# Kernel tuning notes

Measured on AMD Instinct MI355X. Metric: run time of the kernel, lower is better.

## Reference

```python
import jax, jax.numpy as jnp
import numpy as np

T, D_IN, D_OUT, R, S = 8192, 4096, 4096, 16, 16  # tokens, in, out, lora rank, n_stacks
GATE_THRESHOLD = 0.12


def setup_inputs() -> dict:
    key = jax.random.key(0)
    ks = jax.random.split(key, 6)
    x = jax.random.normal(ks[0], (T, D_IN), jnp.float32)
    W = jax.random.normal(ks[1], (D_OUT, D_IN), jnp.float32) * 0.02  # frozen linear weight
    b = jax.random.normal(ks[2], (D_OUT,), jnp.float32) * 0.02       # frozen linear bias
    A = jax.random.normal(ks[3], (S, R, D_IN), jnp.float32) * 0.02   # per-stack lora_A
    B = jax.random.normal(ks[4], (S, D_OUT, R), jnp.float32) * 0.02  # per-stack lora_B
    domain_weights = jax.random.uniform(ks[5], (S,), jnp.float32)    # sigmoid-router weights per domain
    stack_domain = jnp.arange(S, dtype=jnp.int32)                    # stack -> domain index (count=1 each)
    return {"x": x, "W": W, "b": b, "A": A, "B": B,
            "domain_weights": domain_weights, "stack_domain": stack_domain}


def reference(x, W, b, A, B, domain_weights, stack_domain):
    # base frozen linear: out = x @ W^T + b
    base = x @ W.T + b  # [T, D_OUT]
    # threshold-gated per-stack weights: w if w > GATE_THRESHOLD else 0
    g = jnp.where(domain_weights > GATE_THRESHOLD, domain_weights, 0.0)[stack_domain]  # [S]
    # grouped LoRA: stack(x) = (x @ A_s^T) @ B_s^T, combined with gate weights
    h = jnp.einsum('td,srd->str', x, A)          # [S, T, R]
    lora = jnp.einsum('s,str,sor->to', g, h, B)  # [T, D_OUT]
    # original wraps stack contributions in torch.no_grad()
    return base + jax.lax.stop_gradient(lora)
```

## Files before the change

### kernel.cpp

```cpp
#include <hip/hip_runtime.h>
#include <hip/hip_bf16.h>

typedef __bf16 bf16;
typedef __attribute__((ext_vector_type(8))) __bf16 bf16x8;
typedef __attribute__((ext_vector_type(4))) float f32x4;

#define T_TOK 8192
#define DIN   4096
#define DOUT  4096
#define RNK   16
#define NS    16
#define KLORA (NS * RNK)
#define GATE  0.12f

typedef __attribute__((address_space(1))) const void gconst_t;
typedef __attribute__((address_space(3))) void lds_t;

__device__ __forceinline__ void gload_lds16(const void* g, void* l) {
  __builtin_amdgcn_global_load_lds((gconst_t*)g, (lds_t*)l, 16, 0, 0);
}

#define BAR() do { asm volatile("" ::: "memory"); \
                   __builtin_amdgcn_s_barrier();  \
                   asm volatile("" ::: "memory"); } while (0)
#define VMW(n) asm volatile("s_waitcnt vmcnt(" #n ")" ::: "memory")
#define LGKM(n) do { asm volatile("s_waitcnt lgkmcnt(" #n ")" ::: "memory"); \
                     __builtin_amdgcn_sched_barrier(0); } while (0)
#define SB0 __builtin_amdgcn_sched_barrier(0)

__global__ __launch_bounds__(256)
void prep_all_kernel(const float* __restrict__ x, bf16* __restrict__ xb,
                     const float* __restrict__ B, const float* __restrict__ dw,
                     const int* __restrict__ sd, bf16* __restrict__ bg,
                     const float* __restrict__ A, bf16* __restrict__ at) {
  __shared__ float tl[32][33];
  const int bid = blockIdx.x;
  if (bid < 16384) {
    const long i = ((long)bid * 256 + threadIdx.x) * 8;
    const float4 v0 = *(const float4*)(x + i);
    const float4 v1 = *(const float4*)(x + i + 4);
    bf16x8 o;
    o[0] = (bf16)v0.x; o[1] = (bf16)v0.y; o[2] = (bf16)v0.z; o[3] = (bf16)v0.w;
    o[4] = (bf16)v1.x; o[5] = (bf16)v1.y; o[6] = (bf16)v1.z; o[7] = (bf16)v1.w;
    *(bf16x8*)(xb + i) = o;
  } else if (bid < 16384 + 4096) {
    const int t = (bid - 16384) * 256 + threadIdx.x;
    const int o = t >> 8, k = t & 255, s = k >> 4, r = k & 15;
    const float w = dw[sd[s]];
    const float g = (w > GATE) ? w : 0.f;
    bg[t] = (bf16)(g * B[((size_t)s * DOUT + o) * RNK + r]);
  } else {
    const int tb = bid - 16384 - 4096;
    const int d0 = (tb & 127) * 32, k0 = (tb >> 7) * 32;
    const int tx = threadIdx.x & 31, ty = threadIdx.x >> 5;
#pragma unroll
    for (int i = 0; i < 32; i += 8)
      tl[ty + i][tx] = A[(size_t)(k0 + ty + i) * DIN + d0 + tx];
    __syncthreads();
#pragma unroll
    for (int i = 0; i < 32; i += 8)
      at[(size_t)(d0 + ty + i) * KLORA + k0 + tx] = (bf16)tl[tx][ty + i];
  }
}

__global__ __launch_bounds__(256)
void gemm_bt(const bf16* __restrict__ Am, const bf16* __restrict__ Bm,
             const float* __restrict__ extra, bf16* __restrict__ outB,
             int M, int N, int K) {
  constexpr int BM = 128, BN = 128, BK = 32;
  __shared__ __align__(16) bf16 At[BM * BK];
  __shared__ __align__(16) bf16 Bt[BN * BK];

  const int tid  = threadIdx.x;
  const int wave = tid >> 6, lane = tid & 63;

  const int nwg = gridDim.x, bid = blockIdx.x;
  const int qq  = nwg >> 3;
  const int sw  = (bid & 7) * qq + (bid >> 3);
  const int ntN = N / BN;
  const long row0 = (long)(sw / ntN) * BM;
  const long col0 = (long)(sw % ntN) * BN;

  f32x4 acc[4][4] = {};
  const int kSteps = K / BK;

  auto stage = [&](int ks) {
    const long k0 = (long)ks * BK;
#pragma unroll
    for (int r = 0; r < 2; ++r) {
      const int off = tid * 16 + r * 4096;
      const int row = off >> 6;
      const int el  = (off & 63) >> 1;
      char* ldsA = (char*)At + (wave << 10) + (r << 12);
      char* ldsB = (char*)Bt + (wave << 10) + (r << 12);
      gload_lds16(Am + (row0 + row) * K + k0 + el, ldsA);
      gload_lds16(Bm + (col0 + row) * K + k0 + el, ldsB);
    }
  };

  stage(0);
  for (int ks = 0; ks < kSteps; ++ks) {
    __syncthreads();
    bf16x8 afr[4], bfr[4];
    const int koff = (lane >> 4) << 3;
    const int rsel = lane & 15;
    const int wr = wave >> 1, wc = wave & 1;
#pragma unroll
    for (int m = 0; m < 4; ++m)
      afr[m] = *(const bf16x8*)&At[((wr << 6) + (m << 4) + rsel) * BK + koff];
#pragma unroll
    for (int n = 0; n < 4; ++n)
      bfr[n] = *(const bf16x8*)&Bt[((wc << 6) + (n << 4) + rsel) * BK + koff];
    __syncthreads();
    if (ks + 1 < kSteps) stage(ks + 1);
#pragma unroll
    for (int m = 0; m < 4; ++m)
#pragma unroll
      for (int n = 0; n < 4; ++n)
        acc[m][n] = __builtin_amdgcn_mfma_f32_16x16x32_bf16(afr[m], bfr[n],
                                                            acc[m][n], 0, 0, 0);
  }

  const int wr = wave >> 1, wc = wave & 1;
#pragma unroll
  for (int m = 0; m < 4; ++m)
#pragma unroll
    for (int n = 0; n < 4; ++n)
#pragma unroll
      for (int j = 0; j < 4; ++j) {
        const long row = row0 + wr * 64 + m * 16 + ((lane >> 4) << 2) + j;
        const long col = col0 + wc * 64 + n * 16 + (lane & 15);
        outB[row * N + col] = (bf16)(acc[m][n][j] + extra[row * N + col]);
      }
}

__global__ __launch_bounds__(512, 2)
void gemm256(const bf16* __restrict__ Am, const bf16* __restrict__ Bm,
             const float* __restrict__ bias, float* __restrict__ out,
             int M, int N, int K) {
  extern __shared__ char smem[];
  const int tid  = threadIdx.x;
  const int wave = tid >> 6, lane = tid & 63;
  const int wr = wave >> 2, wc = wave & 3;
  const int rsel = lane & 15, klane = lane >> 4;

  const int nwg = gridDim.x, bid = blockIdx.x;
  const int sw  = (bid & 7) * (nwg >> 3) + (bid >> 3);
  const int ntN = N >> 8;
  const long row0 = (long)(sw / ntN) << 8;
  const long col0 = (long)(sw % ntN) << 8;

  long srcA[2], srcB[2];
  int  ldsd[2];
  {
    const int rlo = lane >> 2;
    const int kbe = (((lane & 3) * 16) ^ (((lane >> 5) & 1) << 5)) >> 1;
#pragma unroll
    for (int r = 0; r < 2; ++r) {
      const int row = wave * 32 + r * 16 + rlo;
      srcA[r] = (row0 + row) * (long)K + kbe;
      srcB[r] = (col0 + row) * (long)K + kbe;
      ldsd[r] = (wave * 2 + r) << 10;
    }
  }

  const int nT = K >> 6;

  auto stage_half = [&](int H) {
    if (H >= 4 * nT) return;
    const int  slot = H & 7;
    const long kofs = (long)(H >> 2) * 64 + (long)((H >> 1) & 1) * 32;
    if (H & 1) {
#pragma unroll
      for (int r = 0; r < 2; ++r)
        gload_lds16(Bm + srcB[r] + kofs, smem + (slot << 14) + ldsd[r]);
    } else {
#pragma unroll
      for (int r = 0; r < 2; ++r)
        gload_lds16(Am + srcA[r] + kofs, smem + (slot << 14) + ldsd[r]);
    }
  };

  const int laneoff = rsel * 64 + ((klane * 16) ^ ((rsel & 8) << 2));

  f32x4 acc[8][4] = {};
  bf16x8 afr0[4], afr1[4], bfr0[4], bfr1[4];

#define RDA(slot, mh, mi, dst) \
  (dst)[(mi)] = *(const bf16x8*)(smem + ((slot) << 14) + \
                 (((wr << 7) + (mh) * 64 + (mi) * 16) << 6) + laneoff)
#define RDB(slot, n, dst) \
  (dst)[(n)] = *(const bf16x8*)(smem + ((slot) << 14) + \
                (((wc << 6) + (n) * 16) << 6) + laneoff)
#define MB(mh, mi, A_, B_) do { \
  acc[(mh)*4+(mi)][0] = __builtin_amdgcn_mfma_f32_16x16x32_bf16((A_)[(mi)], (B_)[0], acc[(mh)*4+(mi)][0], 0, 0, 0); \
  acc[(mh)*4+(mi)][1] = __builtin_amdgcn_mfma_f32_16x16x32_bf16((A_)[(mi)], (B_)[1], acc[(mh)*4+(mi)][1], 0, 0, 0); \
  acc[(mh)*4+(mi)][2] = __builtin_amdgcn_mfma_f32_16x16x32_bf16((A_)[(mi)], (B_)[2], acc[(mh)*4+(mi)][2], 0, 0, 0); \
  acc[(mh)*4+(mi)][3] = __builtin_amdgcn_mfma_f32_16x16x32_bf16((A_)[(mi)], (B_)[3], acc[(mh)*4+(mi)][3], 0, 0, 0); \
} while (0)

  stage_half(0); stage_half(1); stage_half(2); stage_half(3); stage_half(4);
  VMW(6);
  BAR();
  RDB(1, 0, bfr0); RDB(1, 1, bfr0); RDB(1, 2, bfr0); RDB(1, 3, bfr0);
  RDA(0, 0, 0, afr0); RDA(0, 0, 1, afr0); RDA(0, 0, 2, afr0); RDA(0, 0, 3, afr0);

  for (int t = 0; t < nT; ++t) {
    const int b  = (t & 1) << 2;
    const int b2 = b ^ 4;
    const bool last = (t == nT - 1);
    BAR();
    stage_half(4 * t + 5);
    LGKM(0);
    __builtin_amdgcn_s_setprio(1);
    MB(0, 0, afr0, bfr0); SB0; RDA(b | 0, 1, 0, afr1); SB0;
    MB(0, 1, afr0, bfr0); SB0; RDA(b | 0, 1, 1, afr1); SB0;
    MB(0, 2, afr0, bfr0); SB0; RDA(b | 0, 1, 2, afr1); SB0;
    MB(0, 3, afr0, bfr0); SB0; RDA(b | 0, 1, 3, afr1);
    __builtin_amdgcn_s_setprio(0);
    if (last) { VMW(0); } else { VMW(4); }
    BAR();
    stage_half(4 * t + 6);
    LGKM(0);
    __builtin_amdgcn_s_setprio(1);
    MB(1, 0, afr1, bfr0); SB0; RDB(b | 3, 0, bfr1); RDB(b | 3, 1, bfr1); SB0;
    MB(1, 1, afr1, bfr0); SB0; RDB(b | 3, 2, bfr1); RDB(b | 3, 3, bfr1); SB0;
    MB(1, 2, afr1, bfr0); SB0; RDA(b | 2, 0, 0, afr0); RDA(b | 2, 0, 1, afr0); SB0;
    MB(1, 3, afr1, bfr0); SB0; RDA(b | 2, 0, 2, afr0); RDA(b | 2, 0, 3, afr0);
    __builtin_amdgcn_s_setprio(0);
    BAR();
    stage_half(4 * t + 7);
    LGKM(0);
    __builtin_amdgcn_s_setprio(1);
    MB(0, 0, afr0, bfr1); SB0; RDA(b | 2, 1, 0, afr1); SB0;
    MB(0, 1, afr0, bfr1); SB0; RDA(b | 2, 1, 1, afr1); SB0;
    MB(0, 2, afr0, bfr1); SB0; RDA(b | 2, 1, 2, afr1); SB0;
    MB(0, 3, afr0, bfr1); SB0; RDA(b | 2, 1, 3, afr1);
    __builtin_amdgcn_s_setprio(0);
    VMW(4);
    BAR();
    stage_half(4 * t + 8);
    LGKM(0);
    __builtin_amdgcn_s_setprio(1);
    if (!last) {
      MB(1, 0, afr1, bfr1); SB0; RDB(b2 | 1, 0, bfr0); RDB(b2 | 1, 1, bfr0); SB0;
      MB(1, 1, afr1, bfr1); SB0; RDB(b2 | 1, 2, bfr0); RDB(b2 | 1, 3, bfr0); SB0;
      MB(1, 2, afr1, bfr1); SB0; RDA(b2 | 0, 0, 0, afr0); RDA(b2 | 0, 0, 1, afr0); SB0;
      MB(1, 3, afr1, bfr1); SB0; RDA(b2 | 0, 0, 2, afr0); RDA(b2 | 0, 0, 3, afr0);
    } else {
      MB(1, 0, afr1, bfr1); MB(1, 1, afr1, bfr1);
      MB(1, 2, afr1, bfr1); MB(1, 3, afr1, bfr1);
    }
    __builtin_amdgcn_s_setprio(0);
  }

#undef RDA
#undef RDB
#undef MB

#pragma unroll
  for (int m = 0; m < 8; ++m)
#pragma unroll
    for (int n = 0; n < 4; ++n)
#pragma unroll
      for (int j = 0; j < 4; ++j) {
        const long row = row0 + wr * 128 + m * 16 + klane * 4 + j;
        const long col = col0 + wc * 64 + n * 16 + rsel;
        out[row * N + col] = acc[m][n][j] + bias[col];
      }
}


extern "C" void kernel_launch(void* const* d_in, const int* in_sizes, int n_in,
                              void* d_out, int out_size, void* d_ws, size_t ws_size,
                              hipStream_t stream) {
  (void)in_sizes; (void)n_in; (void)out_size; (void)ws_size;
  const float* x  = (const float*)d_in[0];
  const float* W  = (const float*)d_in[1];
  const float* b  = (const float*)d_in[2];
  const float* A  = (const float*)d_in[3];
  const float* B  = (const float*)d_in[4];
  const float* dw = (const float*)d_in[5];
  const int*   sd = (const int*)d_in[6];
  float* out = (float*)d_out;

  char* ws = (char*)d_ws;
  bf16* xb    = (bf16*)(ws);
  bf16* weff  = (bf16*)(ws + ((size_t)64 << 20));
  bf16* bg    = (bf16*)(ws + ((size_t)96 << 20));
  bf16* acatT = (bf16*)(ws + ((size_t)98 << 20));

  prep_all_kernel<<<16384 + 4096 + 1024, 256, 0, stream>>>(
      x, xb, B, dw, sd, bg, A, acatT);

  gemm_bt<<<(DOUT / 128) * (DIN / 128), 256, 0, stream>>>(
      bg, acatT, W, weff, DOUT, DIN, KLORA);

  static_assert((T_TOK % 256) == 0 && (DOUT % 256) == 0 && (DIN % 64) == 0, "");
  hipFuncSetAttribute(reinterpret_cast<const void*>(gemm256),
                      hipFuncAttributeMaxDynamicSharedMemorySize, 131072);
  gemm256<<<(T_TOK / 256) * (DOUT / 256), 512, 131072, stream>>>(
      xb, weff, b, out, T_TOK, DOUT, DIN);
}
```

Baseline: 324.5 us.

## Switch main GEMM from 16x16x32 to 32x32x16 bf16 MFMA tiles

Replaces the 16x16x32 MFMA instruction tiling of the 256x256 GEMM with 32x32x16 MFMAs. The LDS swizzle, fragment reads and epilogue indexing are changed to match the 32-row fragment layout. Larger MFMA tiles need fewer LDS fragment reads per FLOP and fewer instructions, which should ease LDS bandwidth and issue pressure. The new swizzle could cause bank conflicts or produce wrong results if it does not match the staging layout.

```diff
diff --git a/kernel.cpp b/kernel.cpp
--- a/kernel.cpp
+++ b/kernel.cpp
@@ -4,6 +4,7 @@
 typedef __bf16 bf16;
 typedef __attribute__((ext_vector_type(8))) __bf16 bf16x8;
 typedef __attribute__((ext_vector_type(4))) float f32x4;
+typedef __attribute__((ext_vector_type(16))) float f32x16;
 
 #define T_TOK 8192
 #define DIN   4096
@@ -142,7 +143,7 @@
   const int tid  = threadIdx.x;
   const int wave = tid >> 6, lane = tid & 63;
   const int wr = wave >> 2, wc = wave & 3;
-  const int rsel = lane & 15, klane = lane >> 4;
+  const int lane31 = lane & 31, kh = lane >> 5;
 
   const int nwg = gridDim.x, bid = blockIdx.x;
   const int sw  = (bid & 7) * (nwg >> 3) + (bid >> 3);
@@ -152,16 +153,13 @@
 
   long srcA[2], srcB[2];
   int  ldsd[2];
-  {
-    const int rlo = lane >> 2;
-    const int kbe = (((lane & 3) * 16) ^ (((lane >> 5) & 1) << 5)) >> 1;
-#pragma unroll
-    for (int r = 0; r < 2; ++r) {
-      const int row = wave * 32 + r * 16 + rlo;
-      srcA[r] = (row0 + row) * (long)K + kbe;
-      srcB[r] = (col0 + row) * (long)K + kbe;
-      ldsd[r] = (wave * 2 + r) << 10;
-    }
+#pragma unroll
+  for (int r = 0; r < 2; ++r) {
+    const int row = wave * 32 + r * 16 + (lane >> 2);
+    const int kbe = ((((lane & 3) * 16) ^ ((lane & 32) >> 1) ^ (r << 5)) >> 1);
+    srcA[r] = (row0 + row) * (long)K + kbe;
+    srcB[r] = (col0 + row) * (long)K + kbe;
+    ldsd[r] = (wave * 2 + r) << 10;
   }
 
   const int nT = K >> 6;
@@ -181,29 +179,31 @@
     }
   };
 
-  const int laneoff = rsel * 64 + ((klane * 16) ^ ((rsel & 8) << 2));
-
-  f32x4 acc[8][4] = {};
-  bf16x8 afr0[4], afr1[4], bfr0[4], bfr1[4];
-
-#define RDA(slot, mh, mi, dst) \
-  (dst)[(mi)] = *(const bf16x8*)(smem + ((slot) << 14) + \
-                 (((wr << 7) + (mh) * 64 + (mi) * 16) << 6) + laneoff)
-#define RDB(slot, n, dst) \
-  (dst)[(n)] = *(const bf16x8*)(smem + ((slot) << 14) + \
-                (((wc << 6) + (n) * 16) << 6) + laneoff)
-#define MB(mh, mi, A_, B_) do { \
-  acc[(mh)*4+(mi)][0] = __builtin_amdgcn_mfma_f32_16x16x32_bf16((A_)[(mi)], (B_)[0], acc[(mh)*4+(mi)][0], 0, 0, 0); \
-  acc[(mh)*4+(mi)][1] = __builtin_amdgcn_mfma_f32_16x16x32_bf16((A_)[(mi)], (B_)[1], acc[(mh)*4+(mi)][1], 0, 0, 0); \
-  acc[(mh)*4+(mi)][2] = __builtin_amdgcn_mfma_f32_16x16x32_bf16((A_)[(mi)], (B_)[2], acc[(mh)*4+(mi)][2], 0, 0, 0); \
-  acc[(mh)*4+(mi)][3] = __builtin_amdgcn_mfma_f32_16x16x32_bf16((A_)[(mi)], (B_)[3], acc[(mh)*4+(mi)][3], 0, 0, 0); \
-} while (0)
+  const int swz = (lane & 24) << 1;
+  int lo32[2];
+  lo32[0] = lane31 * 64 + (((0 * 2 + kh) * 16) ^ swz);
+  lo32[1] = lane31 * 64 + (((1 * 2 + kh) * 16) ^ swz);
+
+  f32x16 acc32[4][2] = {};
+  bf16x8 afr0[2][2], afr1[2][2], bfr0[2][2], bfr1[2][2];
+
+#define RDA32(slot, mh, mi, kst, dst) \
+  (dst)[(mi)][(kst)] = *(const bf16x8*)(smem + ((slot) << 14) + \
+      (((wr << 7) + (mh) * 64 + (mi) * 32) << 6) + lo32[(kst)])
+#define RDB32(slot, n, kst, dst) \
+  (dst)[(n)][(kst)] = *(const bf16x8*)(smem + ((slot) << 14) + \
+      (((wc << 6) + (n) * 32) << 6) + lo32[(kst)])
+#define MB32(mh, mi, n, kst, A_, B_) \
+  acc32[(mh) * 2 + (mi)][(n)] = __builtin_amdgcn_mfma_f32_32x32x16_bf16( \
+      (A_)[(mi)][(kst)], (B_)[(n)][(kst)], acc32[(mh) * 2 + (mi)][(n)], 0, 0, 0)
 
   stage_half(0); stage_half(1); stage_half(2); stage_half(3); stage_half(4);
   VMW(6);
   BAR();
-  RDB(1, 0, bfr0); RDB(1, 1, bfr0); RDB(1, 2, bfr0); RDB(1, 3, bfr0);
-  RDA(0, 0, 0, afr0); RDA(0, 0, 1, afr0); RDA(0, 0, 2, afr0); RDA(0, 0, 3, afr0);
+  RDB32(1, 0, 0, bfr0); RDB32(1, 0, 1, bfr0);
+  RDB32(1, 1, 0, bfr0); RDB32(1, 1, 1, bfr0);
+  RDA32(0, 0, 0, 0, afr0); RDA32(0, 0, 0, 1, afr0);
+  RDA32(0, 0, 1, 0, afr0); RDA32(0, 0, 1, 1, afr0);
 
   for (int t = 0; t < nT; ++t) {
     const int b  = (t & 1) << 2;
@@ -213,29 +213,29 @@
     stage_half(4 * t + 5);
     LGKM(0);
     __builtin_amdgcn_s_setprio(1);
-    MB(0, 0, afr0, bfr0); SB0; RDA(b | 0, 1, 0, afr1); SB0;
-    MB(0, 1, afr0, bfr0); SB0; RDA(b | 0, 1, 1, afr1); SB0;
-    MB(0, 2, afr0, bfr0); SB0; RDA(b | 0, 1, 2, afr1); SB0;
-    MB(0, 3, afr0, bfr0); SB0; RDA(b | 0, 1, 3, afr1);
+    MB32(0, 0, 0, 0, afr0, bfr0); MB32(0, 0, 1, 0, afr0, bfr0); SB0; RDA32(b | 0, 1, 0, 0, afr1); SB0;
+    MB32(0, 1, 0, 0, afr0, bfr0); MB32(0, 1, 1, 0, afr0, bfr0); SB0; RDA32(b | 0, 1, 1, 0, afr1); SB0;
+    MB32(0, 0, 0, 1, afr0, bfr0); MB32(0, 0, 1, 1, afr0, bfr0); SB0; RDA32(b | 0, 1, 0, 1, afr1); SB0;
+    MB32(0, 1, 0, 1, afr0, bfr0); MB32(0, 1, 1, 1, afr0, bfr0); SB0; RDA32(b | 0, 1, 1, 1, afr1);
     __builtin_amdgcn_s_setprio(0);
     if (last) { VMW(0); } else { VMW(4); }
     BAR();
     stage_half(4 * t + 6);
     LGKM(0);
     __builtin_amdgcn_s_setprio(1);
-    MB(1, 0, afr1, bfr0); SB0; RDB(b | 3, 0, bfr1); RDB(b | 3, 1, bfr1); SB0;
-    MB(1, 1, afr1, bfr0); SB0; RDB(b | 3, 2, bfr1); RDB(b | 3, 3, bfr1); SB0;
-    MB(1, 2, afr1, bfr0); SB0; RDA(b | 2, 0, 0, afr0); RDA(b | 2, 0, 1, afr0); SB0;
-    MB(1, 3, afr1, bfr0); SB0; RDA(b | 2, 0, 2, afr0); RDA(b | 2, 0, 3, afr0);
+    MB32(1, 0, 0, 0, afr1, bfr0); MB32(1, 0, 1, 0, afr1, bfr0); SB0; RDB32(b | 3, 0, 0, bfr1); RDB32(b | 3, 0, 1, bfr1); SB0;
+    MB32(1, 1, 0, 0, afr1, bfr0); MB32(1, 1, 1, 0, afr1, bfr0); SB0; RDB32(b | 3, 1, 0, bfr1); RDB32(b | 3, 1, 1, bfr1); SB0;
+    MB32(1, 0, 0, 1, afr1, bfr0); MB32(1, 0, 1, 1, afr1, bfr0); SB0; RDA32(b | 2, 0, 0, 0, afr0); RDA32(b | 2, 0, 0, 1, afr0); SB0;
+    MB32(1, 1, 0, 1, afr1, bfr0); MB32(1, 1, 1, 1, afr1, bfr0); SB0; RDA32(b | 2, 0, 1, 0, afr0); RDA32(b | 2, 0, 1, 1, afr0);
     __builtin_amdgcn_s_setprio(0);
     BAR();
     stage_half(4 * t + 7);
     LGKM(0);
     __builtin_amdgcn_s_setprio(1);
-    MB(0, 0, afr0, bfr1); SB0; RDA(b | 2, 1, 0, afr1); SB0;
-    MB(0, 1, afr0, bfr1); SB0; RDA(b | 2, 1, 1, afr1); SB0;
-    MB(0, 2, afr0, bfr1); SB0; RDA(b | 2, 1, 2, afr1); SB0;
-    MB(0, 3, afr0, bfr1); SB0; RDA(b | 2, 1, 3, afr1);
+    MB32(0, 0, 0, 0, afr0, bfr1); MB32(0, 0, 1, 0, afr0, bfr1); SB0; RDA32(b | 2, 1, 0, 0, afr1); SB0;
+    MB32(0, 1, 0, 0, afr0, bfr1); MB32(0, 1, 1, 0, afr0, bfr1); SB0; RDA32(b | 2, 1, 1, 0, afr1); SB0;
+    MB32(0, 0, 0, 1, afr0, bfr1); MB32(0, 0, 1, 1, afr0, bfr1); SB0; RDA32(b | 2, 1, 0, 1, afr1); SB0;
+    MB32(0, 1, 0, 1, afr0, bfr1); MB32(0, 1, 1, 1, afr0, bfr1); SB0; RDA32(b | 2, 1, 1, 1, afr1);
     __builtin_amdgcn_s_setprio(0);
     VMW(4);
     BAR();
@@ -243,30 +243,32 @@
     LGKM(0);
     __builtin_amdgcn_s_setprio(1);
     if (!last) {
-      MB(1, 0, afr1, bfr1); SB0; RDB(b2 | 1, 0, bfr0); RDB(b2 | 1, 1, bfr0); SB0;
-      MB(1, 1, afr1, bfr1); SB0; RDB(b2 | 1, 2, bfr0); RDB(b2 | 1, 3, bfr0); SB0;
-      MB(1, 2, afr1, bfr1); SB0; RDA(b2 | 0, 0, 0, afr0); RDA(b2 | 0, 0, 1, afr0); SB0;
-      MB(1, 3, afr1, bfr1); SB0; RDA(b2 | 0, 0, 2, afr0); RDA(b2 | 0, 0, 3, afr0);
+      MB32(1, 0, 0, 0, afr1, bfr1); MB32(1, 0, 1, 0, afr1, bfr1); SB0; RDB32(b2 | 1, 0, 0, bfr0); RDB32(b2 | 1, 0, 1, bfr0); SB0;
+      MB32(1, 1, 0, 0, afr1, bfr1); MB32(1, 1, 1, 0, afr1, bfr1); SB0; RDB32(b2 | 1, 1, 0, bfr0); RDB32(b2 | 1, 1, 1, bfr0); SB0;
+      MB32(1, 0, 0, 1, afr1, bfr1); MB32(1, 0, 1, 1, afr1, bfr1); SB0; RDA32(b2 | 0, 0, 0, 0, afr0); RDA32(b2 | 0, 0, 0, 1, afr0); SB0;
+      MB32(1, 1, 0, 1, afr1, bfr1); MB32(1, 1, 1, 1, afr1, bfr1); SB0; RDA32(b2 | 0, 0, 1, 0, afr0); RDA32(b2 | 0, 0, 1, 1, afr0);
     } else {
-      MB(1, 0, afr1, bfr1); MB(1, 1, afr1, bfr1);
-      MB(1, 2, afr1, bfr1); MB(1, 3, afr1, bfr1);
+      MB32(1, 0, 0, 0, afr1, bfr1); MB32(1, 0, 1, 0, afr1, bfr1);
+      MB32(1, 1, 0, 0, afr1, bfr1); MB32(1, 1, 1, 0, afr1, bfr1);
+      MB32(1, 0, 0, 1, afr1, bfr1); MB32(1, 0, 1, 1, afr1, bfr1);
+      MB32(1, 1, 0, 1, afr1, bfr1); MB32(1, 1, 1, 1, afr1, bfr1);
     }
     __builtin_amdgcn_s_setprio(0);
   }
 
-#undef RDA
-#undef RDB
-#undef MB
-
-#pragma unroll
-  for (int m = 0; m < 8; ++m)
-#pragma unroll
-    for (int n = 0; n < 4; ++n)
-#pragma unroll
-      for (int j = 0; j < 4; ++j) {
-        const long row = row0 + wr * 128 + m * 16 + klane * 4 + j;
-        const long col = col0 + wc * 64 + n * 16 + rsel;
-        out[row * N + col] = acc[m][n][j] + bias[col];
+#undef RDA32
+#undef RDB32
+#undef MB32
+
+#pragma unroll
+  for (int mi4 = 0; mi4 < 4; ++mi4)
+#pragma unroll
+    for (int n = 0; n < 2; ++n)
+#pragma unroll
+      for (int reg = 0; reg < 16; ++reg) {
+        const long row = row0 + wr * 128 + mi4 * 32 + (reg & 3) + ((reg >> 2) << 3) + (kh << 2);
+        const long col = col0 + wc * 64 + n * 32 + lane31;
+        out[row * N + col] = acc32[mi4][n][reg] + bias[col];
       }
 }
 
```

Result: no change. 325.6 us (+0.3%).

## Shrink main GEMM tile to 256x128 with triple-buffered K=32 pipeline

Applied to the files above, without the earlier changes.

The main bf16 GEMM moves from a 256x256 output tile with 8 LDS half-slots and a hand-interleaved four-phase schedule to a 256x128 tile. It now uses a 3-stage ring of K=32 slices in 72KB of LDS and a simpler two-phase loop per slice. The smaller LDS and register footprint is meant to raise occupancy (launch bounds 4) and double the number of workgroups. The cost is lower arithmetic intensity per tile, more global traffic for the A operand, more barriers per unit of K, and loss of the finely interleaved MFMA/ds_read scheduling.

```diff
diff --git a/kernel.cpp b/kernel.cpp
--- a/kernel.cpp
+++ b/kernel.cpp
@@ -134,7 +134,7 @@
       }
 }
 
-__global__ __launch_bounds__(512, 2)
+__global__ __launch_bounds__(512, 4)
 void gemm256(const bf16* __restrict__ Am, const bf16* __restrict__ Bm,
              const float* __restrict__ bias, float* __restrict__ out,
              int M, int N, int K) {
@@ -146,112 +146,78 @@
 
   const int nwg = gridDim.x, bid = blockIdx.x;
   const int sw  = (bid & 7) * (nwg >> 3) + (bid >> 3);
-  const int ntN = N >> 8;
+  const int ntN = N >> 7;
   const long row0 = (long)(sw / ntN) << 8;
-  const long col0 = (long)(sw % ntN) << 8;
-
-  long srcA[2], srcB[2];
-  int  ldsd[2];
-  {
-    const int rlo = lane >> 2;
-    const int kbe = (((lane & 3) * 16) ^ (((lane >> 5) & 1) << 5)) >> 1;
-#pragma unroll
-    for (int r = 0; r < 2; ++r) {
-      const int row = wave * 32 + r * 16 + rlo;
-      srcA[r] = (row0 + row) * (long)K + kbe;
-      srcB[r] = (col0 + row) * (long)K + kbe;
-      ldsd[r] = (wave * 2 + r) << 10;
-    }
-  }
-
-  const int nT = K >> 6;
-
-  auto stage_half = [&](int H) {
-    if (H >= 4 * nT) return;
-    const int  slot = H & 7;
-    const long kofs = (long)(H >> 2) * 64 + (long)((H >> 1) & 1) * 32;
-    if (H & 1) {
-#pragma unroll
-      for (int r = 0; r < 2; ++r)
-        gload_lds16(Bm + srcB[r] + kofs, smem + (slot << 14) + ldsd[r]);
-    } else {
-#pragma unroll
-      for (int r = 0; r < 2; ++r)
-        gload_lds16(Am + srcA[r] + kofs, smem + (slot << 14) + ldsd[r]);
-    }
+  const long col0 = (long)(sw % ntN) << 7;
+
+  long srcA[2];
+  int  ldsdA[2];
+#pragma unroll
+  for (int r = 0; r < 2; ++r) {
+    const int row = wave * 32 + r * 16 + (lane >> 2);
+    const int kbe = ((((lane & 3) * 16) ^ (lane & 32)) >> 1);
+    srcA[r] = (row0 + row) * (long)K + kbe;
+    ldsdA[r] = (wave * 2 + r) << 10;
+  }
+  const int rowB = tid >> 2;
+  const int kbeB = ((((lane & 3) * 16) ^ (lane & 32)) >> 1);
+  const long srcB = (col0 + rowB) * (long)K + kbeB;
+  const int  ldsdB = wave << 10;
+
+  const int nS = K >> 5;
+
+  auto stageA = [&](int p, int s2) {
+#pragma unroll
+    for (int r = 0; r < 2; ++r)
+      gload_lds16(Am + srcA[r] + (long)s2 * 32, smem + p * 24576 + ldsdA[r]);
   };
+  auto stageB = [&](int p, int s2) {
+    gload_lds16(Bm + srcB + (long)s2 * 32, smem + p * 24576 + 16384 + ldsdB);
+  };
 
   const int laneoff = rsel * 64 + ((klane * 16) ^ ((rsel & 8) << 2));
 
-  f32x4 acc[8][4] = {};
-  bf16x8 afr0[4], afr1[4], bfr0[4], bfr1[4];
-
-#define RDA(slot, mh, mi, dst) \
-  (dst)[(mi)] = *(const bf16x8*)(smem + ((slot) << 14) + \
-                 (((wr << 7) + (mh) * 64 + (mi) * 16) << 6) + laneoff)
-#define RDB(slot, n, dst) \
-  (dst)[(n)] = *(const bf16x8*)(smem + ((slot) << 14) + \
-                (((wc << 6) + (n) * 16) << 6) + laneoff)
-#define MB(mh, mi, A_, B_) do { \
-  acc[(mh)*4+(mi)][0] = __builtin_amdgcn_mfma_f32_16x16x32_bf16((A_)[(mi)], (B_)[0], acc[(mh)*4+(mi)][0], 0, 0, 0); \
-  acc[(mh)*4+(mi)][1] = __builtin_amdgcn_mfma_f32_16x16x32_bf16((A_)[(mi)], (B_)[1], acc[(mh)*4+(mi)][1], 0, 0, 0); \
-  acc[(mh)*4+(mi)][2] = __builtin_amdgcn_mfma_f32_16x16x32_bf16((A_)[(mi)], (B_)[2], acc[(mh)*4+(mi)][2], 0, 0, 0); \
-  acc[(mh)*4+(mi)][3] = __builtin_amdgcn_mfma_f32_16x16x32_bf16((A_)[(mi)], (B_)[3], acc[(mh)*4+(mi)][3], 0, 0, 0); \
-} while (0)
-
-  stage_half(0); stage_half(1); stage_half(2); stage_half(3); stage_half(4);
-  VMW(6);
+  f32x4 acc[8][2] = {};
+  bf16x8 afr[4], bfr[2];
+
+#define RDA(p, mi, j) \
+  afr[(j)] = *(const bf16x8*)(smem + (p) * 24576 + \
+      (((wr << 7) + (mi) * 16) << 6) + laneoff)
+#define RDB(p, n) \
+  bfr[(n)] = *(const bf16x8*)(smem + (p) * 24576 + 16384 + \
+      (((wc << 5) + (n) * 16) << 6) + laneoff)
+#define MB(mi, j, n) \
+  acc[(mi)][(n)] = __builtin_amdgcn_mfma_f32_16x16x32_bf16( \
+      afr[(j)], bfr[(n)], acc[(mi)][(n)], 0, 0, 0)
+
+  stageB(0, 0); stageA(0, 0);
+  stageB(1, 1); stageA(1, 1);
+  VMW(3);
   BAR();
-  RDB(1, 0, bfr0); RDB(1, 1, bfr0); RDB(1, 2, bfr0); RDB(1, 3, bfr0);
-  RDA(0, 0, 0, afr0); RDA(0, 0, 1, afr0); RDA(0, 0, 2, afr0); RDA(0, 0, 3, afr0);
-
-  for (int t = 0; t < nT; ++t) {
-    const int b  = (t & 1) << 2;
-    const int b2 = b ^ 4;
-    const bool last = (t == nT - 1);
+
+  int p = 0, pst = 2;
+  for (int s = 0; s < nS; ++s) {
+    const bool more = (s + 2 < nS);
+    RDB(p, 0); RDB(p, 1);
+    RDA(p, 0, 0); RDA(p, 1, 1); RDA(p, 2, 2); RDA(p, 3, 3);
+    if (more) stageB(pst, s + 2);
     BAR();
-    stage_half(4 * t + 5);
     LGKM(0);
     __builtin_amdgcn_s_setprio(1);
-    MB(0, 0, afr0, bfr0); SB0; RDA(b | 0, 1, 0, afr1); SB0;
-    MB(0, 1, afr0, bfr0); SB0; RDA(b | 0, 1, 1, afr1); SB0;
-    MB(0, 2, afr0, bfr0); SB0; RDA(b | 0, 1, 2, afr1); SB0;
-    MB(0, 3, afr0, bfr0); SB0; RDA(b | 0, 1, 3, afr1);
+    MB(0, 0, 0); MB(0, 0, 1); MB(1, 1, 0); MB(1, 1, 1);
+    MB(2, 2, 0); MB(2, 2, 1); MB(3, 3, 0); MB(3, 3, 1);
     __builtin_amdgcn_s_setprio(0);
-    if (last) { VMW(0); } else { VMW(4); }
+    RDA(p, 4, 0); RDA(p, 5, 1); RDA(p, 6, 2); RDA(p, 7, 3);
+    if (more) stageA(pst, s + 2);
+    if (s >= nS - 2) { VMW(0); } else { VMW(3); }
     BAR();
-    stage_half(4 * t + 6);
     LGKM(0);
     __builtin_amdgcn_s_setprio(1);
-    MB(1, 0, afr1, bfr0); SB0; RDB(b | 3, 0, bfr1); RDB(b | 3, 1, bfr1); SB0;
-    MB(1, 1, afr1, bfr0); SB0; RDB(b | 3, 2, bfr1); RDB(b | 3, 3, bfr1); SB0;
-    MB(1, 2, afr1, bfr0); SB0; RDA(b | 2, 0, 0, afr0); RDA(b | 2, 0, 1, afr0); SB0;
-    MB(1, 3, afr1, bfr0); SB0; RDA(b | 2, 0, 2, afr0); RDA(b | 2, 0, 3, afr0);
+    MB(4, 0, 0); MB(4, 0, 1); MB(5, 1, 0); MB(5, 1, 1);
+    MB(6, 2, 0); MB(6, 2, 1); MB(7, 3, 0); MB(7, 3, 1);
     __builtin_amdgcn_s_setprio(0);
-    BAR();
-    stage_half(4 * t + 7);
-    LGKM(0);
-    __builtin_amdgcn_s_setprio(1);
-    MB(0, 0, afr0, bfr1); SB0; RDA(b | 2, 1, 0, afr1); SB0;
-    MB(0, 1, afr0, bfr1); SB0; RDA(b | 2, 1, 1, afr1); SB0;
-    MB(0, 2, afr0, bfr1); SB0; RDA(b | 2, 1, 2, afr1); SB0;
-    MB(0, 3, afr0, bfr1); SB0; RDA(b | 2, 1, 3, afr1);
-    __builtin_amdgcn_s_setprio(0);
-    VMW(4);
-    BAR();
-    stage_half(4 * t + 8);
-    LGKM(0);
-    __builtin_amdgcn_s_setprio(1);
-    if (!last) {
-      MB(1, 0, afr1, bfr1); SB0; RDB(b2 | 1, 0, bfr0); RDB(b2 | 1, 1, bfr0); SB0;
-      MB(1, 1, afr1, bfr1); SB0; RDB(b2 | 1, 2, bfr0); RDB(b2 | 1, 3, bfr0); SB0;
-      MB(1, 2, afr1, bfr1); SB0; RDA(b2 | 0, 0, 0, afr0); RDA(b2 | 0, 0, 1, afr0); SB0;
-      MB(1, 3, afr1, bfr1); SB0; RDA(b2 | 0, 0, 2, afr0); RDA(b2 | 0, 0, 3, afr0);
-    } else {
-      MB(1, 0, afr1, bfr1); MB(1, 1, afr1, bfr1);
-      MB(1, 2, afr1, bfr1); MB(1, 3, afr1, bfr1);
-    }
-    __builtin_amdgcn_s_setprio(0);
+    p = (p == 2) ? 0 : p + 1;
+    pst = (pst == 2) ? 0 : pst + 1;
   }
 
 #undef RDA
@@ -259,14 +225,14 @@
 #undef MB
 
 #pragma unroll
-  for (int m = 0; m < 8; ++m)
-#pragma unroll
-    for (int n = 0; n < 4; ++n)
+  for (int mi = 0; mi < 8; ++mi)
+#pragma unroll
+    for (int n = 0; n < 2; ++n)
 #pragma unroll
       for (int j = 0; j < 4; ++j) {
-        const long row = row0 + wr * 128 + m * 16 + klane * 4 + j;
-        const long col = col0 + wc * 64 + n * 16 + rsel;
-        out[row * N + col] = acc[m][n][j] + bias[col];
+        const long row = row0 + wr * 128 + mi * 16 + klane * 4 + j;
+        const long col = col0 + wc * 32 + n * 16 + rsel;
+        out[row * N + col] = acc[mi][n][j] + bias[col];
       }
 }
 
@@ -296,9 +262,9 @@
   gemm_bt<<<(DOUT / 128) * (DIN / 128), 256, 0, stream>>>(
       bg, acatT, W, weff, DOUT, DIN, KLORA);
 
-  static_assert((T_TOK % 256) == 0 && (DOUT % 256) == 0 && (DIN % 64) == 0, "");
+  static_assert((T_TOK % 256) == 0 && (DOUT % 128) == 0 && (DIN % 32) == 0, "");
   hipFuncSetAttribute(reinterpret_cast<const void*>(gemm256),
-                      hipFuncAttributeMaxDynamicSharedMemorySize, 131072);
-  gemm256<<<(T_TOK / 256) * (DOUT / 256), 512, 131072, stream>>>(
+                      hipFuncAttributeMaxDynamicSharedMemorySize, 73728);
+  gemm256<<<(T_TOK / 256) * (DOUT / 128), 512, 73728, stream>>>(
       xb, weff, b, out, T_TOK, DOUT, DIN);
 }
```

Result: slower. 361.7 us (+11.5%).
